# Kernel optimization log

Measured on AMD Instinct MI355X. Metric: run time of the kernel, lower is better.

The kernel has to match this reference:

```python
import jax, jax.numpy as jnp
import numpy as np

BLOCK_SIZE = 32       # MXFP block size (OCP microscaling spec)
E2M1_MAX = 6.0        # max magnitude representable in FP4 E2M1
E2M1_EMAX = 2.0       # exponent of max binade (4..6)


def quantize_mxfp4(t):
    """Fake-quantize t to MXFP4 (E2M1 elements, E8M0 shared scale) along last dim.

    Matches MXFP_F.extract_mxfp_components + dequant: per block of 32 values a
    power-of-two shared scale 2^(floor(log2(amax)) - emax_elem), elements
    rounded to nearest E2M1 value {0, +-0.5, 1, 1.5, 2, 3, 4, 6}.
    """
    shp = t.shape
    tb = t.reshape(shp[:-1] + (shp[-1] // BLOCK_SIZE, BLOCK_SIZE))
    amax = jnp.max(jnp.abs(tb), axis=-1, keepdims=True)
    safe_amax = jnp.where(amax > 0, amax, 1.0)
    shared_exp = jnp.floor(jnp.log2(safe_amax)) - E2M1_EMAX  # E8M0 exponent
    scale = jnp.exp2(shared_exp)
    v = tb / scale
    av = jnp.abs(v)
    # E2M1 grid spacing: 0.5 in [0,2), 1 in [2,4), 2 in [4,6]
    e = jnp.clip(jnp.floor(jnp.log2(jnp.maximum(av, 2.0 ** -10))), 0.0, E2M1_EMAX)
    step = jnp.exp2(e - 1.0)  # one mantissa bit
    q = jnp.clip(jnp.round(av / step) * step, 0.0, E2M1_MAX) * jnp.sign(v)
    return (q * scale).reshape(shp)


def setup_inputs() -> dict:
    key = jax.random.key(0)
    kx, kw, kb = jax.random.split(key, 3)
    B, S, K, N = 2, 4096, 4096, 4096
    x = jax.random.normal(kx, (B, S, K), dtype=jnp.float32)
    weight = jax.random.normal(kw, (N, K), dtype=jnp.float32) * 0.02
    bias = jax.random.normal(kb, (N,), dtype=jnp.float32) * 0.02
    return {"x": x, "weight": weight, "bias": bias}


def reference(x, weight, bias):
    # layer_type 'XqWqB': quantize activations (block along in_features) and
    # weights (block_dim=1 == in_features); bias stays full precision.
    xq = quantize_mxfp4(x)                 # [B, S, K]
    wq = quantize_mxfp4(weight)            # [N, K]
    out = jnp.einsum("bsk,nk->bsn", xq, wq) + bias
    return out
```

## Files before the change

### kernel.cpp

```cpp
#include <hip/hip_runtime.h>
#include <hip/hip_bf16.h>

typedef __attribute__((ext_vector_type(4))) int i32x4;
typedef __attribute__((ext_vector_type(8))) int i32x8;
typedef __attribute__((ext_vector_type(16))) float f32x16;

#define GLOBAL_CPTR(x) ((__attribute__((address_space(1))) const void*)(x))
#define LDS_PTR(x)     ((__attribute__((address_space(3))) void*)(x))

__global__ __launch_bounds__(256) void mxfp4_quant_pack_kernel(
    const float* __restrict__ in, unsigned char* __restrict__ outq,
    unsigned char* __restrict__ outsc, int kshift) {
  const int KC = 1 << (kshift - 5);
  const int CQ = KC >> 2;
  const int bid = blockIdx.x;
  const int cq  = bid & (CQ - 1);
  const int R   = (bid >> (kshift - 7)) << 6;
  const int t   = threadIdx.x;

  __shared__ float sf[64 * 132];

  const float* base = in + ((size_t)R << kshift) + (cq << 7);
#pragma unroll
  for (int i = 0; i < 8; ++i) {
    const int g   = i * 256 + t;
    const int row = g >> 5;
    const int c4  = g & 31;
    float4 v = *reinterpret_cast<const float4*>(
        base + ((size_t)row << kshift) + (c4 << 2));
    *reinterpret_cast<float4*>(sf + row * 132 + (c4 << 2)) = v;
  }
  __syncthreads();

  const int rl = (t & 3) + ((t >> 4) << 2);
  const int kc = (t >> 2) & 3;
  const float* src = sf + rl * 132 + (kc << 5);
  float v[32];
#pragma unroll
  for (int i = 0; i < 8; ++i)
    *reinterpret_cast<float4*>(v + 4 * i) =
        *reinterpret_cast<const float4*>(src + 4 * i);

  float am = 0.f;
#pragma unroll
  for (int j = 0; j < 32; ++j) am = fmaxf(am, fabsf(v[j]));

  const float safe = am > 0.f ? am : 1.f;
  const int se = ilogbf(safe) - 2;
  const float inv = ldexpf(1.f, -se);

  unsigned int packs[4] = {0, 0, 0, 0};
#pragma unroll
  for (int j = 0; j < 32; ++j) {
    const float val = v[j] * inv;
    const float av = fabsf(val);
    const float avc = fmaxf(av, 9.765625e-4f);
    int ee = (int)((__float_as_uint(avc) >> 23) & 0xFF) - 127;
    ee = ee < 0 ? 0 : (ee > 2 ? 2 : ee);
    const float istep = __uint_as_float((unsigned)(128 - ee) << 23);
    const int m = (int)rintf(av * istep);
    unsigned int c = (unsigned)(m + (ee << 1));
    c = c > 7u ? 7u : c;
    c |= (__float_as_uint(val) >> 28) & 8u;
    packs[j >> 3] |= c << (4 * (j & 7));
  }

  const int row = R + rl;
  const size_t chunk = (size_t)(row >> 8) * KC + (cq << 2) + kc;
  *reinterpret_cast<uint4*>(outq + chunk * 4096 + (size_t)(row & 255) * 16) =
      make_uint4(packs[0], packs[1], packs[2], packs[3]);
  outsc[chunk * 256 + (row & 31) * 8 + ((row >> 5) & 7)] =
      (unsigned char)(se + 127);
}

#define BM 256
#define BN 256
#define NTHR 512
#define BUFS 34816

__global__ __launch_bounds__(NTHR, 2) void mxfp_gemm_kernel(
    const unsigned char* __restrict__ Aq, const unsigned char* __restrict__ Asc,
    const unsigned char* __restrict__ Bq, const unsigned char* __restrict__ Bsc,
    const float* __restrict__ bias, float* __restrict__ C,
    int M, int N, int K) {
  __shared__ unsigned char lds[2 * BUFS];

  const int tid = threadIdx.x;
  const int l   = tid & 63;
  const int wid = tid >> 6;
  const int wm  = wid >> 2;
  const int wn  = wid & 3;

  const int nwg = gridDim.x;
  const int bid = blockIdx.x;
  const int swz = (bid & 7) * (nwg >> 3) + (bid >> 3);
  const int nbn = N / BN;
  const int bm  = swz / nbn;
  const int bn  = swz % nbn;

  const int KC = K >> 5;

  f32x16 acc[4][2] = {};

#define STAGE(BUFO, KT)                                                        \
  do {                                                                         \
    const int cl = wid & 3;                                                    \
    const int rg2 = (wid >> 2) << 1;                                           \
    const size_t abase = ((size_t)bm * KC + (size_t)(KT) * 4 + cl) * 4096;     \
    const size_t bbase = ((size_t)bn * KC + (size_t)(KT) * 4 + cl) * 4096;     \
    _Pragma("unroll") for (int i = 0; i < 2; ++i) {                            \
      __builtin_amdgcn_global_load_lds(                                        \
          GLOBAL_CPTR(Aq + abase + (rg2 + i) * 1024 + (l << 4)),               \
          LDS_PTR(lds + (BUFO) + cl * 4096 + (rg2 + i) * 1024), 16, 0, 0);     \
      __builtin_amdgcn_global_load_lds(                                        \
          GLOBAL_CPTR(Bq + bbase + (rg2 + i) * 1024 + (l << 4)),               \
          LDS_PTR(lds + (BUFO) + 16384 + cl * 4096 + (rg2 + i) * 1024),        \
          16, 0, 0);                                                           \
    }                                                                          \
    if (wid < 4) {                                                             \
      __builtin_amdgcn_global_load_lds(                                        \
          GLOBAL_CPTR(Asc + ((size_t)bm * KC + (size_t)(KT) * 4 + wid) * 256   \
                      + (l << 2)),                                             \
          LDS_PTR(lds + (BUFO) + 32768 + wid * 256), 4, 0, 0);                 \
    } else {                                                                   \
      __builtin_amdgcn_global_load_lds(                                        \
          GLOBAL_CPTR(Bsc + ((size_t)bn * KC + (size_t)(KT) * 4 + (wid - 4))   \
                      * 256 + (l << 2)),                                       \
          LDS_PTR(lds + (BUFO) + 33792 + (wid - 4) * 256), 4, 0, 0);           \
    }                                                                          \
  } while (0)

#define KTILE(BUFO)                                                            \
  do {                                                                         \
    const i32x4 z4 = {0, 0, 0, 0};                                             \
    _Pragma("unroll") for (int ks = 0; ks < 2; ++ks) {                         \
      const int cofs = (ks << 13) + ((l & 32) << 7);    \
      i32x8 a8[4], b8[2];                                                      \
      int sa[4], sb[2];                                                        \
      _Pragma("unroll") for (int mb = 0; mb < 4; ++mb)                         \
        a8[mb] = __builtin_shufflevector(                                      \
            *(const i32x4*)(lds + (BUFO) + cofs +                              \
                            (((wm << 7) + (mb << 5) + (l & 31)) << 4)),        \
            z4, 0, 1, 2, 3, 4, 5, 6, 7);                                       \
      _Pragma("unroll") for (int nb = 0; nb < 2; ++nb)                         \
        b8[nb] = __builtin_shufflevector(                                      \
            *(const i32x4*)(lds + (BUFO) + 16384 + cofs +                      \
                            (((wn << 6) + (nb << 5) + (l & 31)) << 4)),        \
            z4, 0, 1, 2, 3, 4, 5, 6, 7);                                       \
      const int av = *(const int*)(lds + (BUFO) + 32768 + (cofs >> 4) +        \
                                   ((l & 31) << 3) + (wm << 2));               \
      const int bv = *(const ushort*)(lds + (BUFO) + 33792 + (cofs >> 4) +     \
                                      ((l & 31) << 3) + (wn << 1));            \
      _Pragma("unroll") for (int mb = 0; mb < 4; ++mb)                         \
        sa[mb] = (int)((unsigned)((av >> (mb << 3)) & 255) * 0x01010101u);     \
      _Pragma("unroll") for (int nb = 0; nb < 2; ++nb)                         \
        sb[nb] = (int)((unsigned)((bv >> (nb << 3)) & 255) * 0x01010101u);     \
      _Pragma("unroll") for (int mb = 0; mb < 4; ++mb)                         \
        _Pragma("unroll") for (int nb = 0; nb < 2; ++nb)                       \
          acc[mb][nb] = __builtin_amdgcn_mfma_scale_f32_32x32x64_f8f6f4(       \
              a8[mb], b8[nb], acc[mb][nb], 4, 4, 0, sa[mb], 0, sb[nb]);        \
    }                                                                          \
  } while (0)

  STAGE(0, 0);
  asm volatile("s_waitcnt vmcnt(0)" ::: "memory");
  __builtin_amdgcn_s_barrier();
  asm volatile("" ::: "memory");

  const int NKT = K >> 7;
  for (int t = 0; t < NKT; ++t) {
    const int tn = (t + 1 < NKT) ? (t + 1) : t;
    const int bufC = (t & 1) ? BUFS : 0;
    const int bufN = (t & 1) ? 0 : BUFS;
    STAGE(bufN, tn);
    KTILE(bufC);
    asm volatile("s_waitcnt vmcnt(0)" ::: "memory");
    __builtin_amdgcn_s_barrier();
    asm volatile("" ::: "memory");
  }

  const int colb = bn * BN + wn * 64 + (l & 31);
  const int rowb = bm * BM + wm * 128 + ((l >> 5) << 2);
  const float bv0 = bias[colb];
  const float bv1 = bias[colb + 32];
#pragma unroll
  for (int mb = 0; mb < 4; ++mb) {
#pragma unroll
    for (int nb = 0; nb < 2; ++nb) {
      const float bv = nb ? bv1 : bv0;
      const int col = colb + nb * 32;
#pragma unroll
      for (int r = 0; r < 16; ++r) {
        const int row = rowb + mb * 32 + ((r >> 2) << 3) + (r & 3);
        C[(size_t)row * N + col] = acc[mb][nb][r] + bv;
      }
    }
  }
}

extern "C" void kernel_launch(void* const* d_in, const int* in_sizes, int n_in,
                              void* d_out, int out_size, void* d_ws, size_t ws_size,
                              hipStream_t stream) {
  const float* x    = (const float*)d_in[0];
  const float* w    = (const float*)d_in[1];
  const float* bias = (const float*)d_in[2];
  float* out = (float*)d_out;

  const int N = in_sizes[2];
  const int K = in_sizes[1] / N;
  const int M = (int)((long long)in_sizes[0] / K);
  const int kshift = __builtin_ctz(K);

  unsigned char* xq  = (unsigned char*)d_ws;
  unsigned char* wq  = xq + ((size_t)M * K >> 1);
  unsigned char* xsc = wq + ((size_t)N * K >> 1);
  unsigned char* wsc = xsc + ((size_t)M * K >> 5);

  const int CQ = (K >> 5) >> 2;

  mxfp4_quant_pack_kernel<<<dim3((unsigned)((M >> 6) * CQ)), dim3(256), 0,
                            stream>>>(x, xq, xsc, kshift);
  mxfp4_quant_pack_kernel<<<dim3((unsigned)((N >> 6) * CQ)), dim3(256), 0,
                            stream>>>(w, wq, wsc, kshift);

  dim3 grid((M / BM) * (N / BN));
  mxfp_gemm_kernel<<<grid, dim3(NTHR), 0, stream>>>(xq, xsc, wq, wsc, bias, out,
                                                    M, N, K);
}
```

Baseline: 140.2 us.

## Deepen GEMM LDS pipeline to four buffers, use MFMA scale opsel, merge quant launches

The GEMM main loop now uses four LDS stages and processes two K-tiles per barrier. It prefetches tiles t+2 and t+3 while computing t and t+1, which halves the barrier and vmcnt waits per K-tile. Per-block scales are now chosen with the MFMA scale opsel byte fields instead of extracting and replicating bytes in VALU code. The activation and weight quantization kernels are merged into one launch that picks its input by block index. The risk is that doubling the LDS footprint to about 136 KB per workgroup likely allows only one workgroup per CU instead of two, which cuts latency hiding.

```diff
diff --git a/kernel.cpp b/kernel.cpp
--- a/kernel.cpp
+++ b/kernel.cpp
@@ -9,11 +9,20 @@
 #define LDS_PTR(x)     ((__attribute__((address_space(3))) void*)(x))
 
 __global__ __launch_bounds__(256) void mxfp4_quant_pack_kernel(
-    const float* __restrict__ in, unsigned char* __restrict__ outq,
-    unsigned char* __restrict__ outsc, int kshift) {
+    const float* __restrict__ xin, unsigned char* __restrict__ xq,
+    unsigned char* __restrict__ xsc, const float* __restrict__ win,
+    unsigned char* __restrict__ wq, unsigned char* __restrict__ wsc,
+    int kshift, int gx) {
   const int KC = 1 << (kshift - 5);
   const int CQ = KC >> 2;
-  const int bid = blockIdx.x;
+  const int bid0 = blockIdx.x;
+  const float* in;
+  unsigned char* outq;
+  unsigned char* outsc;
+  int bid;
+  if (bid0 < gx) { in = xin; outq = xq; outsc = xsc; bid = bid0; }
+  else           { in = win; outq = wq; outsc = wsc; bid = bid0 - gx; }
+
   const int cq  = bid & (CQ - 1);
   const int R   = (bid >> (kshift - 7)) << 6;
   const int t   = threadIdx.x;
@@ -83,7 +92,7 @@
     const unsigned char* __restrict__ Bq, const unsigned char* __restrict__ Bsc,
     const float* __restrict__ bias, float* __restrict__ C,
     int M, int N, int K) {
-  __shared__ unsigned char lds[2 * BUFS];
+  __shared__ unsigned char lds[4 * BUFS];
 
   const int tid = threadIdx.x;
   const int l   = tid & 63;
@@ -130,13 +139,16 @@
     }                                                                          \
   } while (0)
 
+#define MFMA1(MB, NB, AV, BV)                                                  \
+  acc[MB][NB] = __builtin_amdgcn_mfma_scale_f32_32x32x64_f8f6f4(               \
+      a8[MB], b8[NB], acc[MB][NB], 4, 4, MB, AV, NB, BV)
+
 #define KTILE(BUFO)                                                            \
   do {                                                                         \
     const i32x4 z4 = {0, 0, 0, 0};                                             \
     _Pragma("unroll") for (int ks = 0; ks < 2; ++ks) {                         \
       const int cofs = (ks << 13) + ((l & 32) << 7);    \
       i32x8 a8[4], b8[2];                                                      \
-      int sa[4], sb[2];                                                        \
       _Pragma("unroll") for (int mb = 0; mb < 4; ++mb)                         \
         a8[mb] = __builtin_shufflevector(                                      \
             *(const i32x4*)(lds + (BUFO) + cofs +                              \
@@ -151,29 +163,30 @@
                                    ((l & 31) << 3) + (wm << 2));               \
       const int bv = *(const ushort*)(lds + (BUFO) + 33792 + (cofs >> 4) +     \
                                       ((l & 31) << 3) + (wn << 1));            \
-      _Pragma("unroll") for (int mb = 0; mb < 4; ++mb)                         \
-        sa[mb] = (int)((unsigned)((av >> (mb << 3)) & 255) * 0x01010101u);     \
-      _Pragma("unroll") for (int nb = 0; nb < 2; ++nb)                         \
-        sb[nb] = (int)((unsigned)((bv >> (nb << 3)) & 255) * 0x01010101u);     \
-      _Pragma("unroll") for (int mb = 0; mb < 4; ++mb)                         \
-        _Pragma("unroll") for (int nb = 0; nb < 2; ++nb)                       \
-          acc[mb][nb] = __builtin_amdgcn_mfma_scale_f32_32x32x64_f8f6f4(       \
-              a8[mb], b8[nb], acc[mb][nb], 4, 4, 0, sa[mb], 0, sb[nb]);        \
+      MFMA1(0, 0, av, bv); MFMA1(0, 1, av, bv);                                \
+      MFMA1(1, 0, av, bv); MFMA1(1, 1, av, bv);                                \
+      MFMA1(2, 0, av, bv); MFMA1(2, 1, av, bv);                                \
+      MFMA1(3, 0, av, bv); MFMA1(3, 1, av, bv);                                \
     }                                                                          \
   } while (0)
 
   STAGE(0, 0);
+  STAGE(BUFS, 1);
   asm volatile("s_waitcnt vmcnt(0)" ::: "memory");
   __builtin_amdgcn_s_barrier();
   asm volatile("" ::: "memory");
 
   const int NKT = K >> 7;
-  for (int t = 0; t < NKT; ++t) {
-    const int tn = (t + 1 < NKT) ? (t + 1) : t;
-    const int bufC = (t & 1) ? BUFS : 0;
-    const int bufN = (t & 1) ? 0 : BUFS;
-    STAGE(bufN, tn);
-    KTILE(bufC);
+  for (int w = 0; w < (NKT >> 1); ++w) {
+    const int t = w << 1;
+    const int c = (w & 1) ? 2 * BUFS : 0;
+    const int p = (w & 1) ? 0 : 2 * BUFS;
+    const int t2 = (t + 2 < NKT) ? (t + 2) : (NKT - 1);
+    const int t3 = (t + 3 < NKT) ? (t + 3) : (NKT - 1);
+    STAGE(p, t2);
+    KTILE(c);
+    STAGE(p + BUFS, t3);
+    KTILE(c + BUFS);
     asm volatile("s_waitcnt vmcnt(0)" ::: "memory");
     __builtin_amdgcn_s_barrier();
     asm volatile("" ::: "memory");
@@ -217,11 +230,11 @@
   unsigned char* wsc = xsc + ((size_t)M * K >> 5);
 
   const int CQ = (K >> 5) >> 2;
-
-  mxfp4_quant_pack_kernel<<<dim3((unsigned)((M >> 6) * CQ)), dim3(256), 0,
-                            stream>>>(x, xq, xsc, kshift);
-  mxfp4_quant_pack_kernel<<<dim3((unsigned)((N >> 6) * CQ)), dim3(256), 0,
-                            stream>>>(w, wq, wsc, kshift);
+  const int gx = (M >> 6) * CQ;
+  const int gw = (N >> 6) * CQ;
+
+  mxfp4_quant_pack_kernel<<<dim3((unsigned)(gx + gw)), dim3(256), 0, stream>>>(
+      x, xq, xsc, w, wq, wsc, kshift, gx);
 
   dim3 grid((M / BM) * (N / BN));
   mxfp_gemm_kernel<<<grid, dim3(NTHR), 0, stream>>>(xq, xsc, wq, wsc, bias, out,
```

Result: faster. 136.8 us (-2.4%).
